# Kernel tuning notes

Hardware: AMD Instinct MI355X
Metric: run time of the kernel (lower is better)

The kernel has to match this reference:

```python
import jax, jax.numpy as jnp
import numpy as np

C_IN, C_OUT, N, H, W = 128, 256, 3, 256, 256


def im2row(x, n, h, w, c):
    """x: [h*w, c] channel-last pixel-major image -> [(h-n+1)*(w-n+1), c*n*n]
    with each row ordered (channel, ki, kj) to match w.reshape(C_OUT,-1).T."""
    img = x.reshape(h, w, c)
    oh, ow = h - n + 1, w - n + 1
    # stack the n*n shifted views; last axis index = ki*n + kj
    patches = jnp.stack(
        [img[ki:ki + oh, kj:kj + ow, :] for ki in range(n) for kj in range(n)],
        axis=-1,
    )  # [oh, ow, c, n*n]
    return patches.reshape(oh * ow, c * n * n)


def setup_inputs() -> dict:
    key = jax.random.key(0)
    k1, k2, k3, k4 = jax.random.split(key, 4)
    x = jax.random.normal(k1, (H * W, C_IN), dtype=jnp.float32)
    # pre-quantized int8 kernel values (stored as int32), symmetric range
    kernel_q = jax.random.randint(k2, (C_IN * N * N, C_OUT), -127, 128, dtype=jnp.int32)
    kernel_scale = jax.random.uniform(k3, (1,), dtype=jnp.float32, minval=1e-3, maxval=1e-2)
    bias = jax.random.normal(k4, (C_OUT,), dtype=jnp.float32)
    return {"x": x, "kernel_q": kernel_q, "kernel_scale": kernel_scale, "bias": bias}


def reference(x, kernel_q, kernel_scale, bias):
    # im2row unfolding (irregular gather)
    rows = im2row(x, N, H, W, C_IN)                      # [OH*OW, C_IN*N*N]
    # int8 quantized matmul (weights dequantized by per-tensor scale) + bias
    acc = rows @ kernel_q.astype(jnp.float32)            # [OH*OW, C_OUT]
    return acc * kernel_scale + bias
```

## Files before the change

### kernel.cpp

```cpp
#include <hip/hip_runtime.h>
#include <stdint.h>

#define WW 256
#define CIN 128
#define COUT 256
#define OHW 64516
#define KTOT 1152
#define BM 256
#define BK 64
#define NSTEP 18
#define NWG 253
#define BUFSZ 65536

typedef __attribute__((ext_vector_type(8))) short short8;
typedef __attribute__((ext_vector_type(4))) float float4v;
typedef __attribute__((ext_vector_type(4))) float f32x4;
typedef __attribute__((ext_vector_type(4))) unsigned int uint4v;

__device__ __forceinline__ short f2bf(float f) {
    unsigned u = __builtin_bit_cast(unsigned, f);
    unsigned r = u + 0x7fffu + ((u >> 16) & 1u);
    return (short)(r >> 16);
}

__global__ void prep_weights(const int* __restrict__ kq, unsigned short* __restrict__ wt) {
    int o  = blockIdx.x * 256 + threadIdx.x;
    int co = o / KTOT;
    int kp = o - co * KTOT;
    int q  = kp >> 7;
    int c  = kp & 127;
    wt[o] = (unsigned short)f2bf((float)kq[(c * 9 + q) * 256 + co]);
}

__device__ __forceinline__ void gload16(const void* g, void* l) {
    __builtin_amdgcn_global_load_lds(
        (const __attribute__((address_space(1))) unsigned int*)g,
        (__attribute__((address_space(3))) unsigned int*)l, 16, 0, 0);
}

__device__ __forceinline__ unsigned cvtpk(float lo, float hi) {
    unsigned r;
    asm("v_cvt_pk_bf16_f32 %0, %1, %2" : "=v"(r) : "v"(lo), "v"(hi));
    return r;
}

#define SB  __builtin_amdgcn_sched_barrier(0)
#define BAR __builtin_amdgcn_s_barrier()
#define WAIT_VM(n) asm volatile("s_waitcnt vmcnt(" #n ")" ::: "memory")
#define WAIT_LGKM  asm volatile("s_waitcnt lgkmcnt(0)" ::: "memory")

__global__ __launch_bounds__(512, 2) void conv_gemm(
    const float* __restrict__ x,
    const unsigned short* __restrict__ wt,
    const float* __restrict__ scale_p,
    const float* __restrict__ bias,
    float* __restrict__ out)
{
    __shared__ __align__(16) char lds[2 * BUFSZ];

    const int tid  = threadIdx.x;
    const int lane = tid & 63;
    const int wave = tid >> 6;

    const int orig = blockIdx.x;
    const int xcd  = orig & 7;
    const int idx8 = orig >> 3;
    const int wg   = (xcd < 5 ? xcd * 32 : 160 + (xcd - 5) * 31) + idx8;
    const int pbase = wg * BM;

    const int arow  = tid >> 1;
    const int ahalf = tid & 1;
    {
    }
    int p = pbase + arow;
    if (p > OHW - 1) p = OHW - 1;
    const int oy = p / 254;
    const int ox = p - oy * 254;
    const float* abase = x + (oy * WW + ox) * CIN + ahalf * 32;
    int adst[4];
#pragma unroll
    for (int jw = 0; jw < 4; ++jw)
        adst[jw] = arow * 128 + ((ahalf * 64 + jw * 16) ^ ((arow & 7) << 4));

    int bsrc[4];
#pragma unroll
    for (int it = 0; it < 4; ++it) {
        int z    = it * 8192 + wave * 1024 + lane * 16;
        int co   = z >> 7;
        int colb = (z & 127) ^ ((co & 7) << 4);
        bsrc[it] = co * KTOT + (colb >> 1);
    }

    const int wr128 = (wave >> 2) * 128;
    const int wc64  = (wave & 3) * 64;
    const int llo   = lane & 15;
    const int lhi16 = (lane >> 4) * 16;

    f32x4 acc[8][4];
#pragma unroll
    for (int m = 0; m < 8; m++)
#pragma unroll
        for (int n = 0; n < 4; n++) acc[m][n] = (f32x4)0.f;

    float4v fr[8];

#define ISSUE_A(tk) do {                                                        \
    int q_ = (tk) >> 1;  int ki_ = q_ / 3;  int kj_ = q_ - ki_ * 3;             \
    const float* asrc = abase + (ki_ * WW + kj_) * CIN + (((tk) & 1) << 6);     \
    _Pragma("unroll")                                                           \
    for (int j = 0; j < 8; ++j) fr[j] = ((const float4v*)asrc)[j];              \
} while (0)

#define WRITE_A(bufb) do {                                                      \
    _Pragma("unroll")                                                           \
    for (int jw = 0; jw < 4; ++jw) {                                            \
        uint4v U;                                                               \
        U.x = cvtpk(fr[2*jw][0], fr[2*jw][1]);                                  \
        U.y = cvtpk(fr[2*jw][2], fr[2*jw][3]);                                  \
        U.z = cvtpk(fr[2*jw+1][0], fr[2*jw+1][1]);                              \
        U.w = cvtpk(fr[2*jw+1][2], fr[2*jw+1][3]);                              \
        *(uint4v*)(lds + (bufb) + adst[jw]) = U;                                \
    }                                                                           \
} while (0)

#define GLOAD_B(bufb, tk) do {                                                  \
    _Pragma("unroll")                                                           \
    for (int it = 0; it < 4; ++it)                                              \
        gload16(wt + bsrc[it] + (tk) * 64,                                      \
                lds + (bufb) + 32768 + it * 8192 + wave * 1024);                \
} while (0)

#define COMPUTE(bufb) do {                                                      \
    _Pragma("unroll")                                                           \
    for (int kk = 0; kk < 2; ++kk) {                                            \
        short8 bfr[4];                                                          \
        _Pragma("unroll")                                                       \
        for (int n = 0; n < 4; ++n) {                                           \
            int co  = wc64 + n * 16 + llo;                                      \
            int off = co * 128 + ((kk * 64 + lhi16) ^ ((co & 7) << 4));         \
            bfr[n] = *(const short8*)(lds + (bufb) + 32768 + off);              \
        }                                                                       \
        _Pragma("unroll")                                                       \
        for (int mh = 0; mh < 2; ++mh) {                                        \
            short8 af[4];                                                       \
            _Pragma("unroll")                                                   \
            for (int mi = 0; mi < 4; ++mi) {                                    \
                int row = wr128 + mh * 64 + mi * 16 + llo;                      \
                int off = row * 128 + ((kk * 64 + lhi16) ^ ((row & 7) << 4));   \
                af[mi] = *(const short8*)(lds + (bufb) + off);                  \
            }                                                                   \
            __builtin_amdgcn_s_setprio(1);                                      \
            _Pragma("unroll")                                                   \
            for (int mi = 0; mi < 4; ++mi)                                      \
                _Pragma("unroll")                                               \
                for (int n = 0; n < 4; ++n)                                     \
                    acc[mh * 4 + mi][n] = __builtin_amdgcn_mfma_f32_16x16x32_bf16( \
                        af[mi], bfr[n], acc[mh * 4 + mi][n], 0, 0, 0);          \
            __builtin_amdgcn_s_setprio(0);                                      \
        }                                                                       \
    }                                                                           \
} while (0)

    ISSUE_A(0);
    GLOAD_B(0, 0);
    SB; WAIT_VM(4); SB;
    WRITE_A(0);
    ISSUE_A(1);
    GLOAD_B(BUFSZ, 1);
    SB; WAIT_VM(12); SB;
    WAIT_LGKM; SB; BAR; SB;

#pragma unroll 2
    for (int t = 0; t < NSTEP - 2; ++t) {
        const int cur = (t & 1) * BUFSZ;
        const int nxt = cur ^ BUFSZ;
        WRITE_A(nxt);
        COMPUTE(cur);
        WAIT_LGKM; SB; BAR; SB;
        ISSUE_A(t + 2);
        GLOAD_B(cur, t + 2);
        SB; WAIT_VM(12); SB;
        BAR; SB;
    }
    WRITE_A(BUFSZ);
    COMPUTE(0);
    WAIT_LGKM; SB; BAR; SB;
    WAIT_VM(0); SB; BAR; SB;
    COMPUTE(BUFSZ);

    const float scl = scale_p[0];
    const int lhi4 = (lane >> 4) * 4;
#pragma unroll
    for (int n = 0; n < 4; ++n) {
        const int col = wc64 + n * 16 + llo;
        const float bv = bias[col];
#pragma unroll
        for (int m = 0; m < 8; ++m) {
            const int prow = pbase + wr128 + m * 16 + lhi4;
#pragma unroll
            for (int r = 0; r < 4; ++r) {
                const int pp = prow + r;
                if (pp < OHW)
                    out[pp * COUT + col] = acc[m][n][r] * scl + bv;
            }
        }
    }
#undef ISSUE_A
#undef WRITE_A
#undef GLOAD_B
#undef COMPUTE
}

extern "C" void kernel_launch(void* const* d_in, const int* in_sizes, int n_in,
                              void* d_out, int out_size, void* d_ws, size_t ws_size,
                              hipStream_t stream) {
    const float* x     = (const float*)d_in[0];
    const int*   kq    = (const int*)d_in[1];
    const float* scale = (const float*)d_in[2];
    const float* bias  = (const float*)d_in[3];
    float*       out   = (float*)d_out;
    unsigned short* wt = (unsigned short*)d_ws;

    prep_weights<<<KTOT, 256, 0, stream>>>(kq, wt);
    conv_gemm<<<NWG, 512, 0, stream>>>(x, wt, scale, bias, out);
}
```

Measured before the change: 163.5 us.

## Interleave A/B staging with MFMA phases in a four-phase ping-pong schedule

Splits each K-tile's compute into four MFMA phases. Global loads for the next tile, the fp32-to-bf16 conversion and the LDS writes are spread across those phases, separated by barriers. The aim is to hide the A-operand global latency and conversion cost behind matrix work, where before it ran in bulk before compute. The epilogue is also reordered so bias values are loaded once per column and stores are grouped by row. The extra barriers per tile add synchronisation overhead and could stall waves if the phases are unbalanced.

```diff
diff --git a/kernel.cpp b/kernel.cpp
--- a/kernel.cpp
+++ b/kernel.cpp
@@ -70,8 +70,6 @@
 
     const int arow  = tid >> 1;
     const int ahalf = tid & 1;
-    {
-    }
     int p = pbase + arow;
     if (p > OHW - 1) p = OHW - 1;
     const int oy = p / 254;
@@ -103,17 +101,18 @@
         for (int n = 0; n < 4; n++) acc[m][n] = (f32x4)0.f;
 
     float4v fr[8];
-
-#define ISSUE_A(tk) do {                                                        \
+    short8  af[4], bfr[4];
+
+#define ISSUE_A(lo_, tk) do {                                                   \
     int q_ = (tk) >> 1;  int ki_ = q_ / 3;  int kj_ = q_ - ki_ * 3;             \
     const float* asrc = abase + (ki_ * WW + kj_) * CIN + (((tk) & 1) << 6);     \
     _Pragma("unroll")                                                           \
-    for (int j = 0; j < 8; ++j) fr[j] = ((const float4v*)asrc)[j];              \
-} while (0)
-
-#define WRITE_A(bufb) do {                                                      \
-    _Pragma("unroll")                                                           \
-    for (int jw = 0; jw < 4; ++jw) {                                            \
+    for (int j = 0; j < 4; ++j) fr[(lo_) + j] = ((const float4v*)asrc)[(lo_) + j]; \
+} while (0)
+
+#define WRITE_A(bufb, jlo) do {                                                 \
+    _Pragma("unroll")                                                           \
+    for (int jw = (jlo); jw < (jlo) + 2; ++jw) {                                \
         uint4v U;                                                               \
         U.x = cvtpk(fr[2*jw][0], fr[2*jw][1]);                                  \
         U.y = cvtpk(fr[2*jw][2], fr[2*jw][3]);                                  \
@@ -130,85 +129,94 @@
                 lds + (bufb) + 32768 + it * 8192 + wave * 1024);                \
 } while (0)
 
-#define COMPUTE(bufb) do {                                                      \
-    _Pragma("unroll")                                                           \
-    for (int kk = 0; kk < 2; ++kk) {                                            \
-        short8 bfr[4];                                                          \
+#define READ_B(bufb, kk) do {                                                   \
+    _Pragma("unroll")                                                           \
+    for (int n = 0; n < 4; ++n) {                                               \
+        int co  = wc64 + n * 16 + llo;                                          \
+        int off = co * 128 + (((kk) * 64 + lhi16) ^ ((co & 7) << 4));           \
+        bfr[n] = *(const short8*)(lds + (bufb) + 32768 + off);                  \
+    }                                                                           \
+} while (0)
+
+#define READ_A(bufb, mh, kk) do {                                               \
+    _Pragma("unroll")                                                           \
+    for (int mi = 0; mi < 4; ++mi) {                                            \
+        int row = wr128 + (mh) * 64 + mi * 16 + llo;                            \
+        int off = row * 128 + (((kk) * 64 + lhi16) ^ ((row & 7) << 4));         \
+        af[mi] = *(const short8*)(lds + (bufb) + off);                          \
+    }                                                                           \
+} while (0)
+
+#define MFMA16(mh) do {                                                         \
+    __builtin_amdgcn_s_setprio(1);                                              \
+    _Pragma("unroll")                                                           \
+    for (int mi = 0; mi < 4; ++mi)                                              \
         _Pragma("unroll")                                                       \
-        for (int n = 0; n < 4; ++n) {                                           \
-            int co  = wc64 + n * 16 + llo;                                      \
-            int off = co * 128 + ((kk * 64 + lhi16) ^ ((co & 7) << 4));         \
-            bfr[n] = *(const short8*)(lds + (bufb) + 32768 + off);              \
-        }                                                                       \
-        _Pragma("unroll")                                                       \
-        for (int mh = 0; mh < 2; ++mh) {                                        \
-            short8 af[4];                                                       \
-            _Pragma("unroll")                                                   \
-            for (int mi = 0; mi < 4; ++mi) {                                    \
-                int row = wr128 + mh * 64 + mi * 16 + llo;                      \
-                int off = row * 128 + ((kk * 64 + lhi16) ^ ((row & 7) << 4));   \
-                af[mi] = *(const short8*)(lds + (bufb) + off);                  \
-            }                                                                   \
-            __builtin_amdgcn_s_setprio(1);                                      \
-            _Pragma("unroll")                                                   \
-            for (int mi = 0; mi < 4; ++mi)                                      \
-                _Pragma("unroll")                                               \
-                for (int n = 0; n < 4; ++n)                                     \
-                    acc[mh * 4 + mi][n] = __builtin_amdgcn_mfma_f32_16x16x32_bf16( \
-                        af[mi], bfr[n], acc[mh * 4 + mi][n], 0, 0, 0);          \
-            __builtin_amdgcn_s_setprio(0);                                      \
-        }                                                                       \
-    }                                                                           \
-} while (0)
-
-    ISSUE_A(0);
+        for (int n = 0; n < 4; ++n)                                             \
+            acc[(mh) * 4 + mi][n] = __builtin_amdgcn_mfma_f32_16x16x32_bf16(    \
+                af[mi], bfr[n], acc[(mh) * 4 + mi][n], 0, 0, 0);                \
+    __builtin_amdgcn_s_setprio(0);                                              \
+} while (0)
+
+#define TILE(CUR, NXT, TK1, DOSTAGE) do {                                       \
+                                                           \
+    READ_B(CUR, 0); READ_A(CUR, 0, 0);                                          \
+    if (DOSTAGE) { GLOAD_B(NXT, TK1); ISSUE_A(0, TK1); }                        \
+    SB; BAR; WAIT_LGKM; SB; MFMA16(0); SB; BAR; SB;                             \
+                                                           \
+    READ_A(CUR, 1, 0);                                                          \
+    if (DOSTAGE) { ISSUE_A(4, TK1); }                                           \
+    SB; BAR; WAIT_LGKM; SB; MFMA16(1); SB; BAR; SB;                             \
+                                                           \
+    READ_B(CUR, 1); READ_A(CUR, 0, 1);                                          \
+    if (DOSTAGE) { WAIT_VM(4); WRITE_A(NXT, 0); }                               \
+    SB; BAR; WAIT_LGKM; SB; MFMA16(0); SB; BAR; SB;                             \
+                                                           \
+    READ_A(CUR, 1, 1);                                                          \
+    if (DOSTAGE) { WAIT_VM(0); WRITE_A(NXT, 2); }                               \
+    SB; BAR; WAIT_LGKM; SB; MFMA16(1); SB; BAR; SB;                             \
+} while (0)
+
     GLOAD_B(0, 0);
-    SB; WAIT_VM(4); SB;
-    WRITE_A(0);
-    ISSUE_A(1);
-    GLOAD_B(BUFSZ, 1);
-    SB; WAIT_VM(12); SB;
+    ISSUE_A(0, 0);
+    ISSUE_A(4, 0);
+    WAIT_VM(0);
+    WRITE_A(0, 0);
+    WRITE_A(0, 2);
     WAIT_LGKM; SB; BAR; SB;
 
 #pragma unroll 2
-    for (int t = 0; t < NSTEP - 2; ++t) {
-        const int cur = (t & 1) * BUFSZ;
-        const int nxt = cur ^ BUFSZ;
-        WRITE_A(nxt);
-        COMPUTE(cur);
-        WAIT_LGKM; SB; BAR; SB;
-        ISSUE_A(t + 2);
-        GLOAD_B(cur, t + 2);
-        SB; WAIT_VM(12); SB;
-        BAR; SB;
+    for (int t = 0; t < 16; t += 2) {
+        TILE(0,     BUFSZ, t + 1, 1);
+        TILE(BUFSZ, 0,     t + 2, 1);
     }
-    WRITE_A(BUFSZ);
-    COMPUTE(0);
-    WAIT_LGKM; SB; BAR; SB;
-    WAIT_VM(0); SB; BAR; SB;
-    COMPUTE(BUFSZ);
+    TILE(0,     BUFSZ, 17, 1);
+    TILE(BUFSZ, 0,     0,  0);
 
     const float scl = scale_p[0];
     const int lhi4 = (lane >> 4) * 4;
-#pragma unroll
-    for (int n = 0; n < 4; ++n) {
-        const int col = wc64 + n * 16 + llo;
-        const float bv = bias[col];
-#pragma unroll
-        for (int m = 0; m < 8; ++m) {
-            const int prow = pbase + wr128 + m * 16 + lhi4;
-#pragma unroll
-            for (int r = 0; r < 4; ++r) {
-                const int pp = prow + r;
-                if (pp < OHW)
-                    out[pp * COUT + col] = acc[m][n][r] * scl + bv;
+    float bv[4];
+#pragma unroll
+    for (int n = 0; n < 4; ++n) bv[n] = bias[wc64 + n * 16 + llo];
+#pragma unroll
+    for (int m = 0; m < 8; ++m) {
+#pragma unroll
+        for (int r = 0; r < 4; ++r) {
+            const int pp = pbase + wr128 + m * 16 + lhi4 + r;
+            if (pp < OHW) {
+#pragma unroll
+                for (int n = 0; n < 4; ++n)
+                    out[pp * COUT + wc64 + n * 16 + llo] = acc[m][n][r] * scl + bv[n];
             }
         }
     }
 #undef ISSUE_A
 #undef WRITE_A
 #undef GLOAD_B
-#undef COMPUTE
+#undef READ_B
+#undef READ_A
+#undef MFMA16
+#undef TILE
 }
 
 extern "C" void kernel_launch(void* const* d_in, const int* in_sizes, int n_in,
```

Result: faster. 154.8 us (-5.3%).
